# Kernel optimization log

Measured on AMD Instinct MI355X. Metric: run time of the kernel, lower is better.

## Reference

```python
import jax, jax.numpy as jnp
import numpy as np

B, S, V, H, K, T = 4, 256, 32000, 1024, 4, 20
THRESHOLD = 0.6


def setup_inputs() -> dict:
    key = jax.random.key(0)
    ks = jax.random.split(key, 12)
    sH = 1.0 / np.sqrt(H)
    return {
        "input_ids": jax.random.randint(ks[0], (B, S), 0, V),
        "labels": jax.random.randint(ks[1], (B, S), 0, V),
        "embed": jax.random.normal(ks[2], (V, H), jnp.float32) * 0.02,
        "W1": jax.random.normal(ks[3], (H, H), jnp.float32) * sH,
        "b1": jnp.zeros((H,), jnp.float32),
        "lm_head": jax.random.normal(ks[4], (H, V), jnp.float32) * 0.02,
        "W_gen": jax.random.normal(ks[5], (H, H), jnp.float32) * sH,
        "thought_emb": jax.random.normal(ks[6], (K, H), jnp.float32) * 0.02,
        "tpos_emb": jax.random.normal(ks[7], (T, H), jnp.float32) * 0.02,
        "w_score": jax.random.normal(ks[8], (2 * H,), jnp.float32) * sH,
        "w_gate": jax.random.normal(ks[9], (2 * H,), jnp.float32) * sH,
    }


def reference(input_ids, labels, embed, W1, b1, lm_head, W_gen,
              thought_emb, tpos_emb, w_score, w_gate):
    # ---- base model: embed -> tanh MLP -> lm_head ----
    h0 = embed[input_ids]                                 # (B,S,H)
    hidden = jnp.tanh(h0 @ W1 + b1)                       # base last_hidden_state
    base_logits = hidden @ lm_head                        # (B,S,V)

    # ---- ThoughtInjector: per-position gate from normalized entropy ----
    logp = jax.nn.log_softmax(base_logits, axis=-1)
    ent = -jnp.sum(jnp.exp(logp) * logp, axis=-1) / jnp.log(float(V))  # (B,S)
    inject = (ent.mean(axis=0) > THRESHOLD) & (jnp.arange(S) < S - 1)   # (S,)

    # ---- ThoughtGenerator: (B,S,K,T,H) thoughts (masked dispatch, all pos) ----
    g = jnp.tanh(hidden @ W_gen)                          # (B,S,H)
    thoughts = jnp.tanh(g[:, :, None, None, :]
                        + thought_emb[None, None, :, None, :]
                        + tpos_emb[None, None, None, :, :])  # (B,S,K,T,H)
    tmean = thoughts.mean(axis=3)                         # (B,S,K,H) = thoughts.mean(dim=2)

    # ---- CoherenceScorer: composite score per thought ----
    comp = jax.nn.sigmoid(
        jnp.einsum('bsh,h->bs', hidden, w_score[:H])[:, :, None]
        + jnp.einsum('bskh,h->bsk', tmean, w_score[H:]))  # (B,S,K)

    # ---- MixingHead: coherence-weighted thought mix, gated blend with hidden ----
    alpha = jax.nn.softmax(comp, axis=-1)                 # (B,S,K)
    mixed_thought = jnp.einsum('bsk,bskh->bsh', alpha, tmean)
    gate = jax.nn.sigmoid(jnp.einsum('bsh,h->bs', hidden, w_gate[:H])
                          + jnp.einsum('bsh,h->bs', mixed_thought, w_gate[H:]))[..., None]
    mixed = gate * mixed_thought + (1.0 - gate) * hidden

    enhanced = jnp.where(inject[None, :, None], mixed, hidden)
    final_logits = enhanced @ lm_head                     # (B,S,V)

    # ---- shifted cross-entropy loss ----
    sl = jax.nn.log_softmax(final_logits[:, :-1, :], axis=-1)
    loss = -jnp.take_along_axis(sl, labels[:, 1:, None], axis=-1).mean()
    return final_logits, loss
```

## Files before the change

kernel.cpp:

```cpp
#include <hip/hip_runtime.h>


#define V_SZ 32000
#define H_SZ 1024
#define S_SZ 256
#define B_SZ 4
#define M_SZ 1024
#define K_TH 4
#define T_TH 20
#define NTILE_V 250
#define PARTS (NTILE_V * 2)

typedef __bf16 bf16_t;
typedef __bf16 bf16x8 __attribute__((ext_vector_type(8)));
typedef __bf16 bf16x4 __attribute__((ext_vector_type(4)));
typedef float  f32x4  __attribute__((ext_vector_type(4)));

__device__ __forceinline__ float tanh_fast(float x) {
  x = fminf(fmaxf(x, -15.f), 15.f);
  float e = __expf(2.f * x);
  return (e - 1.f) / (e + 1.f);
}
__device__ __forceinline__ float sigmoid_f(float x) {
  return 1.f / (1.f + __expf(-x));
}

__global__ void __launch_bounds__(256) transpose_cast_kernel(
    const float* __restrict__ in, bf16_t* __restrict__ out, int R, int C) {
  __shared__ float tile[32][33];
  const int tx = threadIdx.x & 31, ty = threadIdx.x >> 5;
  const int c0 = blockIdx.x << 5, r0 = blockIdx.y << 5;
  #pragma unroll
  for (int i = ty; i < 32; i += 8)
    tile[i][tx] = in[(size_t)(r0 + i) * C + c0 + tx];
  __syncthreads();
  #pragma unroll
  for (int i = ty; i < 32; i += 8)
    out[(size_t)(c0 + i) * R + r0 + tx] = (bf16_t)tile[tx][i];
}

__global__ void __launch_bounds__(256) gather_cast_kernel(
    const int* __restrict__ ids, const float* __restrict__ embed,
    bf16_t* __restrict__ X0) {
  const int i = blockIdx.x * 256 + threadIdx.x;
  const int m = i >> 8, c4 = (i & 255) << 2;
  const float4 v = *(const float4*)(embed + (size_t)ids[m] * H_SZ + c4);
  bf16x4 o;
  o[0] = (bf16_t)v.x; o[1] = (bf16_t)v.y; o[2] = (bf16_t)v.z; o[3] = (bf16_t)v.w;
  *(bf16x4*)(X0 + (size_t)m * H_SZ + c4) = o;
}

template <int EPI>
__global__ void __launch_bounds__(256, 2) gemm_bt(
    const bf16_t* __restrict__ A, const bf16_t* __restrict__ BT,
    float* __restrict__ outF, bf16_t* __restrict__ outB,
    const float* __restrict__ bias, float2* __restrict__ entP,
    float* __restrict__ lseP, int mtiles, int ntiles, int N) {
  __shared__ __align__(16) bf16_t As[128 * 32];
  __shared__ __align__(16) bf16_t Bs[128 * 32];
  const int t = threadIdx.x;
  const int x = blockIdx.x & 7, y = blockIdx.x >> 3;
  const int tm = y % mtiles, tn = x + 8 * (y / mtiles);
  if (tn >= ntiles) return;
  const int m0 = tm * 128, n0 = tn * 128;
  const int lane = t & 63, wv = t >> 6, wm = wv >> 1, wn = wv & 1;
  const int col = lane & 15, qd = lane >> 4;
  const int ldr = t >> 2, ldch = t & 3;
  const int st0 = ldr * 32 + ((ldch ^ ((ldr >> 1) & 3)) << 3);
  const int st1 = (ldr + 64) * 32 + ((ldch ^ ((ldr >> 1) & 3)) << 3);
  int offA[4], offB[4];
  #pragma unroll
  for (int i = 0; i < 4; ++i) {
    const int ra = wm * 64 + i * 16 + col;
    offA[i] = ra * 32 + ((qd ^ ((ra >> 1) & 3)) << 3);
    const int rb = wn * 64 + i * 16 + col;
    offB[i] = rb * 32 + ((qd ^ ((rb >> 1) & 3)) << 3);
  }
  f32x4 acc[4][4] = {};
  for (int kb = 0; kb < 1024; kb += 32) {
    {
      uint4 a0 = *(const uint4*)(A  + (size_t)(m0 + ldr) * 1024 + kb + ldch * 8);
      uint4 b0 = *(const uint4*)(BT + (size_t)(n0 + ldr) * 1024 + kb + ldch * 8);
      uint4 a1 = *(const uint4*)(A  + (size_t)(m0 + ldr + 64) * 1024 + kb + ldch * 8);
      uint4 b1 = *(const uint4*)(BT + (size_t)(n0 + ldr + 64) * 1024 + kb + ldch * 8);
      *(uint4*)(As + st0) = a0;
      *(uint4*)(Bs + st0) = b0;
      *(uint4*)(As + st1) = a1;
      *(uint4*)(Bs + st1) = b1;
    }
    __syncthreads();
    bf16x8 af[4], bg[4];
    #pragma unroll
    for (int mi = 0; mi < 4; ++mi) af[mi] = *(const bf16x8*)(As + offA[mi]);
    #pragma unroll
    for (int ni = 0; ni < 4; ++ni) bg[ni] = *(const bf16x8*)(Bs + offB[ni]);
    #pragma unroll
    for (int mi = 0; mi < 4; ++mi)
      #pragma unroll
      for (int ni = 0; ni < 4; ++ni)
        acc[mi][ni] = __builtin_amdgcn_mfma_f32_16x16x32_bf16(
            af[mi], bg[ni], acc[mi][ni], 0, 0, 0);
    __syncthreads();
  }

  if (EPI == 3 || EPI == 4) {
    float z[16], s[16];
    #pragma unroll
    for (int mi = 0; mi < 4; ++mi) {
      #pragma unroll
      for (int rr = 0; rr < 4; ++rr) {
        float zz = 0.f, ss = 0.f;
        #pragma unroll
        for (int ni = 0; ni < 4; ++ni) {
          const float xv = acc[mi][ni][rr];
          const float e = __expf(xv);
          zz += e;
          if (EPI == 3) ss += xv * e;
          if (EPI == 4) {
            const size_t o = (size_t)(m0 + wm * 64 + mi * 16 + qd * 4 + rr) * N
                           + (n0 + wn * 64 + ni * 16 + col);
            outF[o] = xv;
          }
        }
        z[mi * 4 + rr] = zz;
        s[mi * 4 + rr] = ss;
      }
    }
    #pragma unroll
    for (int d = 1; d < 16; d <<= 1) {
      #pragma unroll
      for (int i = 0; i < 16; ++i) {
        z[i] += __shfl_xor(z[i], d);
        if (EPI == 3) s[i] += __shfl_xor(s[i], d);
      }
    }
    if (col == 0) {
      #pragma unroll
      for (int i = 0; i < 16; ++i) {
        const int row = m0 + wm * 64 + (i >> 2) * 16 + qd * 4 + (i & 3);
        if (EPI == 3)
          entP[(size_t)row * PARTS + tn * 2 + wn] = make_float2(z[i], s[i]);
        else
          lseP[(size_t)row * PARTS + tn * 2 + wn] = z[i];
      }
    }
    return;
  }

  #pragma unroll
  for (int mi = 0; mi < 4; ++mi) {
    #pragma unroll
    for (int ni = 0; ni < 4; ++ni) {
      const int gm = m0 + wm * 64 + mi * 16 + qd * 4;
      const int gn = n0 + wn * 64 + ni * 16 + col;
      #pragma unroll
      for (int r = 0; r < 4; ++r) {
        const size_t o = (size_t)(gm + r) * N + gn;
        float v = acc[mi][ni][r];
        if (EPI == 1) {
          v = tanh_fast(v + bias[gn]);
          outF[o] = v;
          outB[o] = (bf16_t)v;
        } else if (EPI == 2) {
          outF[o] = tanh_fast(v);
        } else {
          outF[o] = v;
        }
      }
    }
  }
}

__global__ void __launch_bounds__(256) ent_inject_kernel(
    const float2* __restrict__ entP, int* __restrict__ inject) {
  const int s = blockIdx.x, t = threadIdx.x;
  const int b = t >> 6, lane = t & 63;
  const int row = b * S_SZ + s;
  float z = 0.f, sv = 0.f;
  for (int i = lane; i < PARTS; i += 64) {
    const float2 p = entP[(size_t)row * PARTS + i];
    z += p.x; sv += p.y;
  }
  #pragma unroll
  for (int d = 1; d < 64; d <<= 1) {
    z += __shfl_xor(z, d);
    sv += __shfl_xor(sv, d);
  }
  __shared__ float se[4];
  if (lane == 0) se[b] = __logf(z) - sv / z;
  __syncthreads();
  if (t == 0) {
    const float e = 0.25f * (se[0] + se[1] + se[2] + se[3]);
    inject[s] = (e * (1.0f / 10.373491f) > 0.6f) && (s < S_SZ - 1) ? 1 : 0;
  }
}

__global__ void __launch_bounds__(256) lse_merge_kernel(
    const float* __restrict__ lseP, float* __restrict__ lse) {
  const int t = threadIdx.x, w = t >> 6, lane = t & 63;
  const int row = blockIdx.x * 4 + w;
  float z = 0.f;
  for (int i = lane; i < PARTS; i += 64) z += lseP[(size_t)row * PARTS + i];
  #pragma unroll
  for (int d = 1; d < 64; d <<= 1) z += __shfl_xor(z, d);
  if (lane == 0) lse[row] = __logf(z);
}

__global__ void __launch_bounds__(256) thoughts_kernel(
    const float* __restrict__ g, const float* __restrict__ th_emb,
    const float* __restrict__ tpos, float* __restrict__ tmean) {
  const int idx = blockIdx.x * 256 + threadIdx.x;
  const int h = idx & (H_SZ - 1);
  const int mk = idx >> 10;
  const int kk = mk & (K_TH - 1);
  const int m = mk >> 2;
  const float base = g[(size_t)m * H_SZ + h] + th_emb[kk * H_SZ + h];
  float s = 0.f;
  #pragma unroll
  for (int tt = 0; tt < T_TH; ++tt) s += tanh_fast(base + tpos[tt * H_SZ + h]);
  tmean[idx] = s * (1.f / T_TH);
}

__device__ __forceinline__ float block_sum(float v, float* red, int t) {
  red[t] = v;
  __syncthreads();
  for (int off = 128; off > 0; off >>= 1) {
    if (t < off) red[t] += red[t + off];
    __syncthreads();
  }
  const float r = red[0];
  __syncthreads();
  return r;
}

__global__ void __launch_bounds__(256) mix_kernel(
    const float* __restrict__ hidden, const float* __restrict__ tmean,
    const float* __restrict__ w_score, const float* __restrict__ w_gate,
    const int* __restrict__ inject, bf16_t* __restrict__ enhB) {
  const int m = blockIdx.x, t = threadIdx.x, s = m & (S_SZ - 1);
  __shared__ float red[256];
  float hv[4], ws1[4], ws2[4], wg1[4], wg2[4], tmv[4][4];
  #pragma unroll
  for (int j = 0; j < 4; ++j) {
    const int h = t + 256 * j;
    hv[j]  = hidden[(size_t)m * H_SZ + h];
    ws1[j] = w_score[h];      ws2[j] = w_score[H_SZ + h];
    wg1[j] = w_gate[h];       wg2[j] = w_gate[H_SZ + h];
    #pragma unroll
    for (int k = 0; k < 4; ++k) tmv[k][j] = tmean[(size_t)(m * 4 + k) * H_SZ + h];
  }
  float ph = 0.f, pg = 0.f;
  #pragma unroll
  for (int j = 0; j < 4; ++j) { ph += hv[j] * ws1[j]; pg += hv[j] * wg1[j]; }
  const float sh = block_sum(ph, red, t);
  const float gh = block_sum(pg, red, t);
  float comp[4];
  #pragma unroll
  for (int k = 0; k < 4; ++k) {
    float pc = 0.f;
    #pragma unroll
    for (int j = 0; j < 4; ++j) pc += tmv[k][j] * ws2[j];
    const float ck = block_sum(pc, red, t);
    comp[k] = sigmoid_f(sh + ck);
  }
  const float ma = fmaxf(fmaxf(comp[0], comp[1]), fmaxf(comp[2], comp[3]));
  float al[4], asum = 0.f;
  #pragma unroll
  for (int k = 0; k < 4; ++k) { al[k] = __expf(comp[k] - ma); asum += al[k]; }
  const float inv = 1.f / asum;
  float mx[4];
  #pragma unroll
  for (int j = 0; j < 4; ++j) {
    mx[j] = 0.f;
    #pragma unroll
    for (int k = 0; k < 4; ++k) mx[j] += al[k] * inv * tmv[k][j];
  }
  float pm = 0.f;
  #pragma unroll
  for (int j = 0; j < 4; ++j) pm += mx[j] * wg2[j];
  const float gm = block_sum(pm, red, t);
  const float gate = sigmoid_f(gh + gm);
  const int inj = inject[s];
  #pragma unroll
  for (int j = 0; j < 4; ++j) {
    const float e = inj ? (gate * mx[j] + (1.f - gate) * hv[j]) : hv[j];
    enhB[(size_t)m * H_SZ + t + 256 * j] = (bf16_t)e;
  }
}

__global__ void __launch_bounds__(256) loss_kernel(
    const float* __restrict__ logits, const float* __restrict__ lse,
    const int* __restrict__ labels, float* __restrict__ out_loss) {
  const int t = threadIdx.x;
  float acc = 0.f;
  for (int i = t; i < (S_SZ - 1) * B_SZ; i += 256) {
    const int b = i / (S_SZ - 1), s2 = i % (S_SZ - 1);
    const int m = b * S_SZ + s2;
    const int lab = labels[m + 1];
    acc += lse[m] - logits[(size_t)m * V_SZ + lab];
  }
  __shared__ float red[256];
  red[t] = acc;
  __syncthreads();
  for (int off = 128; off > 0; off >>= 1) {
    if (t < off) red[t] += red[t + off];
    __syncthreads();
  }
  if (t == 0) out_loss[0] = red[0] / (float)((S_SZ - 1) * B_SZ);
}

extern "C" void kernel_launch(void* const* d_in, const int* in_sizes, int n_in,
                              void* d_out, int out_size, void* d_ws, size_t ws_size,
                              hipStream_t stream) {
  const int*   ids    = (const int*)  d_in[0];
  const int*   labels = (const int*)  d_in[1];
  const float* embed  = (const float*)d_in[2];
  const float* W1     = (const float*)d_in[3];
  const float* b1     = (const float*)d_in[4];
  const float* lm     = (const float*)d_in[5];
  const float* Wg     = (const float*)d_in[6];
  const float* thE    = (const float*)d_in[7];
  const float* tpos   = (const float*)d_in[8];
  const float* wsc    = (const float*)d_in[9];
  const float* wgt    = (const float*)d_in[10];
  float* out = (float*)d_out;

  char* p = (char*)d_ws;
  auto carve = [&p](size_t bytes) {
    char* r = p;
    p += (bytes + 255) & ~(size_t)255;
    return r;
  };
  bf16_t* lmT   = (bf16_t*)carve((size_t)V_SZ * H_SZ * sizeof(bf16_t));
  bf16_t* W1T   = (bf16_t*)carve((size_t)H_SZ * H_SZ * sizeof(bf16_t));
  bf16_t* WgT   = (bf16_t*)carve((size_t)H_SZ * H_SZ * sizeof(bf16_t));
  bf16_t* X0    = (bf16_t*)carve((size_t)M_SZ * H_SZ * sizeof(bf16_t));
  bf16_t* hidB  = (bf16_t*)carve((size_t)M_SZ * H_SZ * sizeof(bf16_t));
  bf16_t* enhB  = (bf16_t*)carve((size_t)M_SZ * H_SZ * sizeof(bf16_t));
  float*  hidF  = (float*) carve((size_t)M_SZ * H_SZ * sizeof(float));
  float*  gF    = (float*) carve((size_t)M_SZ * H_SZ * sizeof(float));
  float*  tmean = (float*) carve((size_t)M_SZ * K_TH * H_SZ * sizeof(float));
  float*  lse   = (float*) carve(M_SZ * sizeof(float));
  int*    inj   = (int*)   carve(S_SZ * sizeof(int));
  float2* entP = (float2*)tmean;
  float*  lseP = (float*)tmean;

  transpose_cast_kernel<<<dim3(V_SZ / 32, H_SZ / 32), 256, 0, stream>>>(lm, lmT, H_SZ, V_SZ);
  transpose_cast_kernel<<<dim3(H_SZ / 32, H_SZ / 32), 256, 0, stream>>>(W1, W1T, H_SZ, H_SZ);
  transpose_cast_kernel<<<dim3(H_SZ / 32, H_SZ / 32), 256, 0, stream>>>(Wg, WgT, H_SZ, H_SZ);
  gather_cast_kernel<<<M_SZ * H_SZ / 4 / 256, 256, 0, stream>>>(ids, embed, X0);

  gemm_bt<1><<<64, 256, 0, stream>>>(X0, W1T, hidF, hidB, b1, nullptr, nullptr, 8, 8, H_SZ);
  gemm_bt<2><<<64, 256, 0, stream>>>(hidB, WgT, gF, nullptr, nullptr, nullptr, nullptr, 8, 8, H_SZ);
  gemm_bt<3><<<2048, 256, 0, stream>>>(hidB, lmT, nullptr, nullptr, nullptr, entP, nullptr, 8, NTILE_V, V_SZ);
  ent_inject_kernel<<<S_SZ, 256, 0, stream>>>(entP, inj);

  thoughts_kernel<<<M_SZ * K_TH * H_SZ / 256, 256, 0, stream>>>(gF, thE, tpos, tmean);
  mix_kernel<<<M_SZ, 256, 0, stream>>>(hidF, tmean, wsc, wgt, inj, enhB);

  gemm_bt<4><<<2048, 256, 0, stream>>>(enhB, lmT, out, nullptr, nullptr, nullptr, lseP, 8, NTILE_V, V_SZ);
  lse_merge_kernel<<<M_SZ / 4, 256, 0, stream>>>(lseP, lse);
  loss_kernel<<<1, 256, 0, stream>>>(out, lse, labels, out + (size_t)M_SZ * V_SZ);
}
```

Measured before the change: 602.0 us.

## Use async global-to-LDS loads in GEMM, fuse thoughts into mix, widen transpose

The GEMM tile loads now go through global_load_lds, which copies straight from global memory into LDS instead of staging through registers, with per-wave contiguous LDS destinations and swizzle folded into the global address. The separate thoughts kernel is removed; mix_kernel computes the tanh means in registers, so the 16MB tmean buffer is no longer written and read back. The transpose-cast kernel uses 64x64 tiles with float4 loads and 8-wide bf16 stores. Risks: still a single LDS buffer with no prefetch overlap, and the LDS layout written by the async copy has to match the swizzled read offsets exactly.

```diff
diff --git a/kernel.cpp b/kernel.cpp
--- a/kernel.cpp
+++ b/kernel.cpp
@@ -16,6 +16,13 @@
 typedef __bf16 bf16x4 __attribute__((ext_vector_type(4)));
 typedef float  f32x4  __attribute__((ext_vector_type(4)));
 
+typedef __attribute__((address_space(1))) void gvoid_t;
+typedef __attribute__((address_space(3))) void lvoid_t;
+
+__device__ __forceinline__ void async_copy16(const bf16_t* g, bf16_t* l) {
+  __builtin_amdgcn_global_load_lds((gvoid_t*)g, (lvoid_t*)l, 16, 0, 0);
+}
+
 __device__ __forceinline__ float tanh_fast(float x) {
   x = fminf(fmaxf(x, -15.f), 15.f);
   float e = __expf(2.f * x);
@@ -27,16 +34,27 @@
 
 __global__ void __launch_bounds__(256) transpose_cast_kernel(
     const float* __restrict__ in, bf16_t* __restrict__ out, int R, int C) {
-  __shared__ float tile[32][33];
-  const int tx = threadIdx.x & 31, ty = threadIdx.x >> 5;
-  const int c0 = blockIdx.x << 5, r0 = blockIdx.y << 5;
-  #pragma unroll
-  for (int i = ty; i < 32; i += 8)
-    tile[i][tx] = in[(size_t)(r0 + i) * C + c0 + tx];
-  __syncthreads();
-  #pragma unroll
-  for (int i = ty; i < 32; i += 8)
-    out[(size_t)(c0 + i) * R + r0 + tx] = (bf16_t)tile[tx][i];
+  __shared__ float tile[64][65];
+  const int t = threadIdx.x;
+  const int c0 = blockIdx.x << 6, r0 = blockIdx.y << 6;
+  const int tr = t >> 4, tc = (t & 15) << 2;
+  #pragma unroll
+  for (int i = 0; i < 4; ++i) {
+    const float4 v = *(const float4*)(in + (size_t)(r0 + tr + 16 * i) * C + c0 + tc);
+    tile[tr + 16 * i][tc]     = v.x;
+    tile[tr + 16 * i][tc + 1] = v.y;
+    tile[tr + 16 * i][tc + 2] = v.z;
+    tile[tr + 16 * i][tc + 3] = v.w;
+  }
+  __syncthreads();
+  const int wr = t >> 3, wc = (t & 7) << 3;
+  #pragma unroll
+  for (int i = 0; i < 2; ++i) {
+    bf16x8 o;
+    #pragma unroll
+    for (int j = 0; j < 8; ++j) o[j] = (bf16_t)tile[wc + j][wr + 32 * i];
+    *(bf16x8*)(out + (size_t)(c0 + wr + 32 * i) * R + r0 + wc) = o;
+  }
 }
 
 __global__ void __launch_bounds__(256) gather_cast_kernel(
@@ -65,9 +83,18 @@
   const int m0 = tm * 128, n0 = tn * 128;
   const int lane = t & 63, wv = t >> 6, wm = wv >> 1, wn = wv & 1;
   const int col = lane & 15, qd = lane >> 4;
-  const int ldr = t >> 2, ldch = t & 3;
-  const int st0 = ldr * 32 + ((ldch ^ ((ldr >> 1) & 3)) << 3);
-  const int st1 = (ldr + 64) * 32 + ((ldch ^ ((ldr >> 1) & 3)) << 3);
+
+  const int srow = 16 * wv + (lane >> 2);
+  const int schunk = ((lane & 3) ^ ((srow >> 1) & 3)) << 3;
+  const bf16_t* gA0 = A  + (size_t)(m0 + srow) * 1024 + schunk;
+  const bf16_t* gA1 = A  + (size_t)(m0 + srow + 64) * 1024 + schunk;
+  const bf16_t* gB0 = BT + (size_t)(n0 + srow) * 1024 + schunk;
+  const bf16_t* gB1 = BT + (size_t)(n0 + srow + 64) * 1024 + schunk;
+  bf16_t* lA0 = As + wv * 512;
+  bf16_t* lA1 = As + 2048 + wv * 512;
+  bf16_t* lB0 = Bs + wv * 512;
+  bf16_t* lB1 = Bs + 2048 + wv * 512;
+
   int offA[4], offB[4];
   #pragma unroll
   for (int i = 0; i < 4; ++i) {
@@ -78,16 +105,10 @@
   }
   f32x4 acc[4][4] = {};
   for (int kb = 0; kb < 1024; kb += 32) {
-    {
-      uint4 a0 = *(const uint4*)(A  + (size_t)(m0 + ldr) * 1024 + kb + ldch * 8);
-      uint4 b0 = *(const uint4*)(BT + (size_t)(n0 + ldr) * 1024 + kb + ldch * 8);
-      uint4 a1 = *(const uint4*)(A  + (size_t)(m0 + ldr + 64) * 1024 + kb + ldch * 8);
-      uint4 b1 = *(const uint4*)(BT + (size_t)(n0 + ldr + 64) * 1024 + kb + ldch * 8);
-      *(uint4*)(As + st0) = a0;
-      *(uint4*)(Bs + st0) = b0;
-      *(uint4*)(As + st1) = a1;
-      *(uint4*)(Bs + st1) = b1;
-    }
+    async_copy16(gA0 + kb, lA0);
+    async_copy16(gA1 + kb, lA1);
+    async_copy16(gB0 + kb, lB0);
+    async_copy16(gB1 + kb, lB1);
     __syncthreads();
     bf16x8 af[4], bg[4];
     #pragma unroll
@@ -206,21 +227,6 @@
   if (lane == 0) lse[row] = __logf(z);
 }
 
-__global__ void __launch_bounds__(256) thoughts_kernel(
-    const float* __restrict__ g, const float* __restrict__ th_emb,
-    const float* __restrict__ tpos, float* __restrict__ tmean) {
-  const int idx = blockIdx.x * 256 + threadIdx.x;
-  const int h = idx & (H_SZ - 1);
-  const int mk = idx >> 10;
-  const int kk = mk & (K_TH - 1);
-  const int m = mk >> 2;
-  const float base = g[(size_t)m * H_SZ + h] + th_emb[kk * H_SZ + h];
-  float s = 0.f;
-  #pragma unroll
-  for (int tt = 0; tt < T_TH; ++tt) s += tanh_fast(base + tpos[tt * H_SZ + h]);
-  tmean[idx] = s * (1.f / T_TH);
-}
-
 __device__ __forceinline__ float block_sum(float v, float* red, int t) {
   red[t] = v;
   __syncthreads();
@@ -234,7 +240,8 @@
 }
 
 __global__ void __launch_bounds__(256) mix_kernel(
-    const float* __restrict__ hidden, const float* __restrict__ tmean,
+    const float* __restrict__ hidden, const float* __restrict__ gF,
+    const float* __restrict__ th_emb, const float* __restrict__ tpos,
     const float* __restrict__ w_score, const float* __restrict__ w_gate,
     const int* __restrict__ inject, bf16_t* __restrict__ enhB) {
   const int m = blockIdx.x, t = threadIdx.x, s = m & (S_SZ - 1);
@@ -246,8 +253,18 @@
     hv[j]  = hidden[(size_t)m * H_SZ + h];
     ws1[j] = w_score[h];      ws2[j] = w_score[H_SZ + h];
     wg1[j] = w_gate[h];       wg2[j] = w_gate[H_SZ + h];
-    #pragma unroll
-    for (int k = 0; k < 4; ++k) tmv[k][j] = tmean[(size_t)(m * 4 + k) * H_SZ + h];
+    const float gv = gF[(size_t)m * H_SZ + h];
+    float tp[T_TH];
+    #pragma unroll
+    for (int tt = 0; tt < T_TH; ++tt) tp[tt] = tpos[tt * H_SZ + h];
+    #pragma unroll
+    for (int k = 0; k < 4; ++k) {
+      const float base = gv + th_emb[k * H_SZ + h];
+      float ssum = 0.f;
+      #pragma unroll
+      for (int tt = 0; tt < T_TH; ++tt) ssum += tanh_fast(base + tp[tt]);
+      tmv[k][j] = ssum * (1.f / T_TH);
+    }
   }
   float ph = 0.f, pg = 0.f;
   #pragma unroll
@@ -339,15 +356,15 @@
   bf16_t* enhB  = (bf16_t*)carve((size_t)M_SZ * H_SZ * sizeof(bf16_t));
   float*  hidF  = (float*) carve((size_t)M_SZ * H_SZ * sizeof(float));
   float*  gF    = (float*) carve((size_t)M_SZ * H_SZ * sizeof(float));
-  float*  tmean = (float*) carve((size_t)M_SZ * K_TH * H_SZ * sizeof(float));
+  float*  partials = (float*)carve((size_t)M_SZ * PARTS * sizeof(float2));
   float*  lse   = (float*) carve(M_SZ * sizeof(float));
   int*    inj   = (int*)   carve(S_SZ * sizeof(int));
-  float2* entP = (float2*)tmean;
-  float*  lseP = (float*)tmean;
-
-  transpose_cast_kernel<<<dim3(V_SZ / 32, H_SZ / 32), 256, 0, stream>>>(lm, lmT, H_SZ, V_SZ);
-  transpose_cast_kernel<<<dim3(H_SZ / 32, H_SZ / 32), 256, 0, stream>>>(W1, W1T, H_SZ, H_SZ);
-  transpose_cast_kernel<<<dim3(H_SZ / 32, H_SZ / 32), 256, 0, stream>>>(Wg, WgT, H_SZ, H_SZ);
+  float2* entP = (float2*)partials;
+  float*  lseP = (float*)partials;
+
+  transpose_cast_kernel<<<dim3(V_SZ / 64, H_SZ / 64), 256, 0, stream>>>(lm, lmT, H_SZ, V_SZ);
+  transpose_cast_kernel<<<dim3(H_SZ / 64, H_SZ / 64), 256, 0, stream>>>(W1, W1T, H_SZ, H_SZ);
+  transpose_cast_kernel<<<dim3(H_SZ / 64, H_SZ / 64), 256, 0, stream>>>(Wg, WgT, H_SZ, H_SZ);
   gather_cast_kernel<<<M_SZ * H_SZ / 4 / 256, 256, 0, stream>>>(ids, embed, X0);
 
   gemm_bt<1><<<64, 256, 0, stream>>>(X0, W1T, hidF, hidB, b1, nullptr, nullptr, 8, 8, H_SZ);
@@ -355,8 +372,7 @@
   gemm_bt<3><<<2048, 256, 0, stream>>>(hidB, lmT, nullptr, nullptr, nullptr, entP, nullptr, 8, NTILE_V, V_SZ);
   ent_inject_kernel<<<S_SZ, 256, 0, stream>>>(entP, inj);
 
-  thoughts_kernel<<<M_SZ * K_TH * H_SZ / 256, 256, 0, stream>>>(gF, thE, tpos, tmean);
-  mix_kernel<<<M_SZ, 256, 0, stream>>>(hidF, tmean, wsc, wgt, inj, enhB);
+  mix_kernel<<<M_SZ, 256, 0, stream>>>(hidF, gF, thE, tpos, wsc, wgt, inj, enhB);
 
   gemm_bt<4><<<2048, 256, 0, stream>>>(enhB, lmT, out, nullptr, nullptr, nullptr, lseP, 8, NTILE_V, V_SZ);
   lse_merge_kernel<<<M_SZ / 4, 256, 0, stream>>>(lseP, lse);
```

After: 618.7 us. 2.8% more time.
